# Performance work log

Measured on AMD Instinct MI355X. Metric: run time of the kernel, lower is better.

## Reference

```python
import jax, jax.numpy as jnp
import numpy as np

LOG2PI = float(np.log(2.0 * np.pi))

# Each Gaussian g is exp(-0.5*(a_g.x + b_g.y + c_g)^2)/sqrt(2*pi), with x the H current
# hidden variables and y the H next hidden variables. The original module applies a
# precompiled sequence of Givens-rotation 'gaussian products' (sequence_phase_1/2) that
# (phase 1) zero the x-coefficients of all but one pivot Gaussian per variable and
# integrate the pivots out, then (phase 2) rotate the leftover Gaussians so only H of
# them depend on y; leftover pure-bias Gaussians contribute norm_log_gaussian(bias).
# A sequence of Givens rotations is an orthogonal transform of the rows [a|b|c], so the
# whole procedure equals (up to per-row signs, which leave every Gaussian invariant):
#   QR on A -> integrate H pivots: LC1 = -sum_j log|R1_jj|
#   project B,c onto A's orthogonal complement, QR on PB -> kept rows (R2, Q2^T Pc)
#   residual bias energy -> LC2 = -0.5*((K-H)*log(2pi) + ||(P - Q2 Q2^T) c||^2)


def setup_inputs() -> dict:
    B, P, H, K, D = 2048, 4, 16, 48, 4
    key = jax.random.key(0)
    ks = jax.random.split(key, 8)
    f32 = jnp.float32
    return {
        "input_i": jax.random.normal(ks[0], (B, P, D), dtype=f32),
        "Prev_coefs": jax.random.normal(ks[1], (H, B, P, H), dtype=f32),
        "Prev_biases": jax.random.normal(ks[2], (H, B, P), dtype=f32),
        "LP": jnp.zeros((B, P), dtype=f32),
        "Log_factors": jax.random.normal(ks[3], (B, P), dtype=f32),
        "obs_var_coefs": jax.random.normal(ks[4], (K, B, P, D), dtype=f32),
        "hidden_var_coefs": jax.random.normal(ks[5], (K, B, P, H), dtype=f32),
        "next_hidden_var_coefs": jax.random.normal(ks[6], (K, B, P, H), dtype=f32),
        "rec_biases": jax.random.normal(ks[7], (K, B, P), dtype=f32),
    }


def reference(input_i, Prev_coefs, Prev_biases, LP, Log_factors,
              obs_var_coefs, hidden_var_coefs, next_hidden_var_coefs, rec_biases):
    H = Prev_coefs.shape[0]
    K = rec_biases.shape[0]
    # observation contribution to the recurrent Gaussians' biases: [K,B,P]
    cur_b = rec_biases + jnp.sum(obs_var_coefs * input_i[None], axis=-1)
    # stack all G = H + K Gaussians: coefs on current hidden vars (A), next hidden
    # vars (Bm) and biases (c). Previous-step Gaussians have zero next-var coefs.
    A = jnp.concatenate([Prev_coefs, hidden_var_coefs], axis=0)            # [G,B,P,H]
    Bm = jnp.concatenate([jnp.zeros_like(Prev_coefs), next_hidden_var_coefs], 0)
    c = jnp.concatenate([Prev_biases, cur_b], axis=0)                      # [G,B,P]
    A = jnp.moveaxis(A, 0, 2)   # [B,P,G,H]
    Bm = jnp.moveaxis(Bm, 0, 2)  # [B,P,G,H]
    c = jnp.moveaxis(c, 0, 2)   # [B,P,G]

    # phase 1: orthogonal elimination of the current-hidden-variable coefficients,
    # then integrate the H pivot Gaussians out.
    Q1, R1 = jnp.linalg.qr(A)                                              # Q1 [B,P,G,H]
    diag1 = jnp.abs(jnp.diagonal(R1, axis1=-2, axis2=-1))
    LC = -jnp.sum(jnp.log(diag1), axis=-1)                                 # [B,P]
    # project next-var coefs and biases onto the orthogonal complement of span(A)
    PB = Bm - Q1 @ (jnp.swapaxes(Q1, -1, -2) @ Bm)                         # [B,P,G,H]
    Pc = c - jnp.einsum('bpgh,bph->bpg', Q1, jnp.einsum('bpgh,bpg->bph', Q1, c))

    # phase 2: reduce the remaining K Gaussians to H kept ones.
    Q2, R2 = jnp.linalg.qr(PB)                                             # R2 [B,P,H,H]
    nb = jnp.einsum('bpgh,bpg->bph', Q2, Pc)                               # kept biases
    resid = jnp.maximum(jnp.sum(Pc * Pc, -1) - jnp.sum(nb * nb, -1), 0.0)
    # leftover (K - H) pure-bias Gaussians: sum of norm_log_gaussian(bias)
    LC = LC - 0.5 * ((K - H) * LOG2PI + resid)

    LP_new = LP + LC + Log_factors
    Next_coefs = jnp.moveaxis(R2, 2, 0)    # [H,B,P,H]
    Next_biases = jnp.moveaxis(nb, -1, 0)  # [H,B,P]
    return (Next_coefs, Next_biases, LP_new)
```

## Files before the change

kernel.cpp:

```cpp
#include <hip/hip_runtime.h>

#define LOG2PI 1.8378770664093453

__device__ __forceinline__ float rl32(float v, int l) {
  return __int_as_float(__builtin_amdgcn_readlane(__float_as_int(v), l));
}

#define OFF_M33   0
#define OFF_STAB  1188
#define OFF_T     1188
#define OFF_Y     1508
#define OFF_Z     1828
#define OFF_G     2148
#define OFF_CTOP  2454
#define OFF_ATOPT 2470
#define OFF_M2    2790
#define LDSZ      2792

__device__ __forceinline__ void slot_to_rq(int s, int& r, int& q) {
  if      (s < 4)   { r = s;               q = 0;    }
  else if (s < 12)  { int i=s-4;   r=4 +i/2; q=i-(i/2)*2; }
  else if (s < 24)  { int i=s-12;  r=8 +i/3; q=i-(i/3)*3; }
  else if (s < 40)  { int i=s-24;  r=12+(i>>2); q=i&3; }
  else if (s < 60)  { int i=s-40;  r=16+i/5; q=i-(i/5)*5; }
  else if (s < 84)  { int i=s-60;  r=20+i/6; q=i-(i/6)*6; }
  else if (s < 112) { int i=s-84;  r=24+i/7; q=i-(i/7)*7; }
  else if (s < 144) { int i=s-112; r=28+(i>>3); q=i&7; }
  else              { r = 32; q = s-144; }
}

__global__ __launch_bounds__(128, 7) void cint_kernel(
    const float* __restrict__ input_i,
    const float* __restrict__ Prev_coefs,
    const float* __restrict__ Prev_biases,
    const float* __restrict__ LPin,
    const float* __restrict__ Log_factors,
    const float* __restrict__ obs_var,
    const float* __restrict__ hid_var,
    const float* __restrict__ nxt_var,
    const float* __restrict__ rec_biases,
    float* __restrict__ out,
    int NBP)
{
  __shared__ float lds[LDSZ];

  const int tid  = threadIdx.x;
  const int w    = tid >> 6;
  const int lane = tid & 63;
  const int bid  = blockIdx.x;
  const int inst = (bid & 7) * (NBP >> 3) + (bid >> 3);

  const size_t NB_OFFv = (size_t)NBP * 256;
  const size_t LP_OFFv = NB_OFFv + (size_t)NBP * 16;

  const float lp_lf = LPin[inst] + Log_factors[inst];

  {
    const int g = lane;
    const size_t rowidx = (g < 16) ? ((size_t)g * NBP + inst)
                                   : ((size_t)(g - 16) * NBP + inst);
    if (w == 0) {
      const float* aptr = (g < 16) ? (Prev_coefs + rowidx * 16)
                                   : (hid_var    + rowidx * 16);
      float4 a0 = *(const float4*)(aptr + 0);
      float4 a1 = *(const float4*)(aptr + 4);
      float4 a2 = *(const float4*)(aptr + 8);
      float4 a3 = *(const float4*)(aptr + 12);
      *(float4*)&lds[g*36 +  0] = a0;
      *(float4*)&lds[g*36 +  4] = a1;
      *(float4*)&lds[g*36 +  8] = a2;
      *(float4*)&lds[g*36 + 12] = a3;
      if (g < 16) {
        lds[OFF_ATOPT +  0*20+g]=a0.x; lds[OFF_ATOPT +  1*20+g]=a0.y;
        lds[OFF_ATOPT +  2*20+g]=a0.z; lds[OFF_ATOPT +  3*20+g]=a0.w;
        lds[OFF_ATOPT +  4*20+g]=a1.x; lds[OFF_ATOPT +  5*20+g]=a1.y;
        lds[OFF_ATOPT +  6*20+g]=a1.z; lds[OFF_ATOPT +  7*20+g]=a1.w;
        lds[OFF_ATOPT +  8*20+g]=a2.x; lds[OFF_ATOPT +  9*20+g]=a2.y;
        lds[OFF_ATOPT + 10*20+g]=a2.z; lds[OFF_ATOPT + 11*20+g]=a2.w;
        lds[OFF_ATOPT + 12*20+g]=a3.x; lds[OFF_ATOPT + 13*20+g]=a3.y;
        lds[OFF_ATOPT + 14*20+g]=a3.z; lds[OFF_ATOPT + 15*20+g]=a3.w;
      }
    } else {
      float4 z4 = make_float4(0.f, 0.f, 0.f, 0.f);
      float4 b0 = z4, b1 = z4, b2 = z4, b3 = z4;
      float cv;
      if (g < 16) {
        cv = Prev_biases[rowidx];
        lds[OFF_CTOP + g] = cv;
      } else {
        const float* bptr = nxt_var + rowidx * 16;
        b0 = *(const float4*)(bptr + 0);
        b1 = *(const float4*)(bptr + 4);
        b2 = *(const float4*)(bptr + 8);
        b3 = *(const float4*)(bptr + 12);
        float4 ob = *(const float4*)(obs_var + rowidx * 4);
        float4 iv = *(const float4*)(input_i + (size_t)inst * 4);
        cv = rec_biases[rowidx] + ob.x*iv.x + ob.y*iv.y + ob.z*iv.z + ob.w*iv.w;
      }
      *(float4*)&lds[g*36 + 16] = b0;
      *(float4*)&lds[g*36 + 20] = b1;
      *(float4*)&lds[g*36 + 24] = b2;
      *(float4*)&lds[g*36 + 28] = b3;
      lds[g*36 + 32] = cv;
      lds[g*36 + 33] = 0.f; lds[g*36 + 34] = 0.f; lds[g*36 + 35] = 0.f;
    }
  }
  __syncthreads();

  int r0, q0; slot_to_rq(tid, r0, q0);
  float a00=0,a01=0,a02=0,a03=0;
  {
    #pragma unroll 8
    for (int g = 0; g < 64; ++g) {
      const float* xr = &lds[g*36];
      float  xi = xr[r0];
      float4 cv = *(const float4*)(xr + 4*q0);
      a00=fmaf(xi,cv.x,a00); a01=fmaf(xi,cv.y,a01);
      a02=fmaf(xi,cv.z,a02); a03=fmaf(xi,cv.w,a03);
    }
  }
  const bool has2 = (tid >= 103);
  int r1=0, q1=0;
  float a10=0,a11=0,a12=0,a13=0;
  if (has2) {
    slot_to_rq(tid + 25, r1, q1);
    #pragma unroll 8
    for (int g = 0; g < 64; ++g) {
      const float* xr = &lds[g*36];
      float  xi = xr[r1];
      float4 cv = *(const float4*)(xr + 4*q1);
      a10=fmaf(xi,cv.x,a10); a11=fmaf(xi,cv.y,a11);
      a12=fmaf(xi,cv.z,a12); a13=fmaf(xi,cv.w,a13);
    }
  }
  __syncthreads();

  {
    float4 v0 = make_float4(a00,a01,a02,a03);
    *(float4*)&lds[OFF_M33 + r0*36 + 4*q0] = v0;
    if (r0 >= 16 && q0 < 4) {
      const int k = r0 - 16;
      lds[OFF_STAB + (4*q0+0)*20 + k] = a00;
      lds[OFF_STAB + (4*q0+1)*20 + k] = a01;
      lds[OFF_STAB + (4*q0+2)*20 + k] = a02;
      lds[OFF_STAB + (4*q0+3)*20 + k] = a03;
    }
    if (has2) {
      float4 v1 = make_float4(a10,a11,a12,a13);
      *(float4*)&lds[OFF_M33 + r1*36 + 4*q1] = v1;
      if (r1 >= 16 && q1 < 4) {
        const int k = r1 - 16;
        lds[OFF_STAB + (4*q1+0)*20 + k] = a10;
        lds[OFF_STAB + (4*q1+1)*20 + k] = a11;
        lds[OFF_STAB + (4*q1+2)*20 + k] = a12;
        lds[OFF_STAB + (4*q1+3)*20 + k] = a13;
      }
    }
  }
  __syncthreads();

  if (w == 0) {
    float Lr[16];
    {
      const int ir = lane & 15;
      double prodd = 1.0;
      #pragma unroll
      for (int j = 0; j < 16; ++j) {
        float s = lds[OFF_M33 + ((ir >= j) ? (ir*36 + j) : (j*36 + ir))];
        #pragma unroll
        for (int m = 0; m < j; ++m) s = fmaf(-Lr[m], rl32(Lr[m], j), s);
        float sj = fmaxf(rl32(s, j), 1e-30f);
        float Ljj = sqrtf(sj);
        float iv  = 1.0f / Ljj;
        prodd *= (double)sj;
        Lr[j] = (ir == j) ? Ljj : s * iv;
        if (lane == j) lds[OFF_M33 + j*36 + 33] = iv;
      }
      if (lane == 0) lds[OFF_M2 + 1] = (float)(-0.5 * log(prodd));
    }
    {
      const bool isY = (lane < 17);
      const int  ci  = isY ? lane : ((lane - 17 < 15) ? lane - 17 : 15);
      const float* ip = isY ? &lds[OFF_STAB + ci] : &lds[OFF_ATOPT + ci];
      float x[16];
      #pragma unroll
      for (int j = 0; j < 16; ++j) {
        float t = ip[j*20];
        #pragma unroll
        for (int m = 0; m < j; ++m) t = fmaf(-rl32(Lr[m], j), x[m], t);
        x[j] = t * lds[OFF_M33 + j*36 + 33];
      }
      if (lane < 33) {
        float* op = isY ? &lds[OFF_Y + ci] : &lds[OFF_Z + ci];
        #pragma unroll
        for (int m = 0; m < 16; ++m) op[m*20] = x[m];
      }
    }
  }
  __syncthreads();

  for (int s = tid; s < 153; s += 128) {
    float fs = 8.f * (float)s + 1.f;
    int k = (int)((sqrtf(fs) - 1.f) * 0.5f);
    int l = s - ((k * (k + 1)) >> 1);
    float acc = lds[OFF_M33 + (16 + k)*36 + 16 + l];
    #pragma unroll
    for (int m = 0; m < 16; ++m)
      acc = fmaf(-lds[OFF_Y + m*20 + k], lds[OFF_Y + m*20 + l], acc);
    lds[OFF_G + k*18 + l] = acc;
    lds[OFF_G + l*18 + k] = acc;
  }
  {
    #pragma unroll
    for (int p = 0; p < 4; ++p) {
      int s = p * 128 + tid;
      int r  = s >> 5;
      int kk = s & 31;
      if (kk < 17) {
        float acc = (kk == 16) ? lds[OFF_CTOP + r] : 0.f;
        #pragma unroll
        for (int m = 0; m < 16; ++m)
          acc = fmaf(-lds[OFF_Z + m*20 + r], lds[OFF_Y + m*20 + kk], acc);
        lds[OFF_T + r*20 + kk] = acc;
      }
    }
  }
  __syncthreads();

  if (w == 0) {
    const int k  = lane;
    const int kc = (k < 17) ? k : 16;
    float Tr[16];
    float Gh[16];
    #pragma unroll
    for (int r = 0; r < 16; ++r) Tr[r] = lds[OFF_T + r*20 + kc];
    #pragma unroll
    for (int j = 0; j < 16; ++j) Gh[j] = lds[OFF_G + j*18 + kc];
    float nbacc = 0.0f;
    #pragma unroll
    for (int j = 0; j < 16; ++j) {
      float alf  = rl32(Tr[j], j);
      float nrm2 = rl32(Gh[j], j);
      float nrm  = sqrtf(fmaxf(nrm2, 1e-30f));
      float aa   = fabsf(alf);
      float tau  = 1.0f + aa / nrm;
      float inv  = copysignf(1.0f / (aa + nrm), alf);
      float beta = -copysignf(nrm, alf);
      float Tj   = Tr[j];
      float wv   = Tj + (Gh[j] - alf * Tj) * inv;
      float Rv   = Tj - tau * wv;
      if (k < 16) {
        float ov = (k < j) ? 0.0f : ((k == j) ? beta : Rv);
        out[((size_t)j * NBP + inst) * 16 + k] = ov;
      } else if (k == 16) {
        out[NB_OFFv + (size_t)j * NBP + inst] = Rv;
        nbacc = fmaf(Rv, Rv, nbacc);
      }
      float twi = tau * wv * inv;
      #pragma unroll
      for (int r = j + 1; r < 16; ++r) {
        float vr = rl32(Tr[r], j);
        Tr[r] = fmaf(-twi, vr, Tr[r]);
      }
      #pragma unroll
      for (int l = j + 1; l < 16; ++l) {
        float Rl = rl32(Rv, l);
        Gh[l] = fmaf(-Rl, Rv, Gh[l]);
      }
    }
    if (k == 16) {
      double resid = fmax((double)lds[OFF_G + 16*18 + 16] - (double)nbacc, 0.0);
      double LC = (double)lds[OFF_M2 + 1] - 0.5 * (32.0 * LOG2PI + resid);
      out[LP_OFFv + (size_t)inst] = lp_lf + (float)LC;
    }
  }
}

extern "C" void kernel_launch(void* const* d_in, const int* in_sizes, int n_in,
                              void* d_out, int out_size, void* d_ws, size_t ws_size,
                              hipStream_t stream) {
  (void)n_in; (void)out_size; (void)d_ws; (void)ws_size;
  const int NBP = in_sizes[3];
  cint_kernel<<<NBP, 128, 0, stream>>>(
      (const float*)d_in[0], (const float*)d_in[1], (const float*)d_in[2],
      (const float*)d_in[3], (const float*)d_in[4], (const float*)d_in[5],
      (const float*)d_in[6], (const float*)d_in[7], (const float*)d_in[8],
      (float*)d_out, NBP);
}
```

Measured before the change: 177.0 us.

## Collapse per-instance block to a single wavefront and drop all barriers

Each instance is now handled by one 64-lane wavefront instead of two, so every __syncthreads is removed. Each lane computes up to three Gram-matrix slots instead of one or two. The LDS layout is compacted by reusing the Gram region for the T and G intermediates and reading transposed inputs in place instead of staging copies. The intent is to cut barrier and idle-wave overhead, at the cost of more serial work per wave, lower launch_bounds occupancy and correctness that now depends on lockstep wave execution for LDS visibility.

```diff
diff --git a/kernel.cpp b/kernel.cpp
--- a/kernel.cpp
+++ b/kernel.cpp
@@ -6,16 +6,11 @@
   return __int_as_float(__builtin_amdgcn_readlane(__float_as_int(v), l));
 }
 
-#define OFF_M33   0
-#define OFF_STAB  1188
-#define OFF_T     1188
-#define OFF_Y     1508
-#define OFF_Z     1828
-#define OFF_G     2148
-#define OFF_CTOP  2454
-#define OFF_ATOPT 2470
-#define OFF_M2    2790
-#define LDSZ      2792
+#define MO   1116
+#define YO   2304
+#define ZO   2576
+#define LC1O (MO + 34)
+#define WSZ  2848
 
 __device__ __forceinline__ void slot_to_rq(int s, int& r, int& q) {
   if      (s < 4)   { r = s;               q = 0;    }
@@ -29,7 +24,7 @@
   else              { r = 32; q = s-144; }
 }
 
-__global__ __launch_bounds__(128, 7) void cint_kernel(
+__global__ __launch_bounds__(64, 4) void cint_kernel(
     const float* __restrict__ input_i,
     const float* __restrict__ Prev_coefs,
     const float* __restrict__ Prev_biases,
@@ -42,11 +37,9 @@
     float* __restrict__ out,
     int NBP)
 {
-  __shared__ float lds[LDSZ];
-
-  const int tid  = threadIdx.x;
-  const int w    = tid >> 6;
-  const int lane = tid & 63;
+  __shared__ float L[WSZ];
+
+  const int lane = threadIdx.x;
   const int bid  = blockIdx.x;
   const int inst = (bid & 7) * (NBP >> 3) + (bid >> 3);
 
@@ -57,185 +50,134 @@
 
   {
     const int g = lane;
-    const size_t rowidx = (g < 16) ? ((size_t)g * NBP + inst)
-                                   : ((size_t)(g - 16) * NBP + inst);
-    if (w == 0) {
-      const float* aptr = (g < 16) ? (Prev_coefs + rowidx * 16)
-                                   : (hid_var    + rowidx * 16);
-      float4 a0 = *(const float4*)(aptr + 0);
-      float4 a1 = *(const float4*)(aptr + 4);
-      float4 a2 = *(const float4*)(aptr + 8);
-      float4 a3 = *(const float4*)(aptr + 12);
-      *(float4*)&lds[g*36 +  0] = a0;
-      *(float4*)&lds[g*36 +  4] = a1;
-      *(float4*)&lds[g*36 +  8] = a2;
-      *(float4*)&lds[g*36 + 12] = a3;
-      if (g < 16) {
-        lds[OFF_ATOPT +  0*20+g]=a0.x; lds[OFF_ATOPT +  1*20+g]=a0.y;
-        lds[OFF_ATOPT +  2*20+g]=a0.z; lds[OFF_ATOPT +  3*20+g]=a0.w;
-        lds[OFF_ATOPT +  4*20+g]=a1.x; lds[OFF_ATOPT +  5*20+g]=a1.y;
-        lds[OFF_ATOPT +  6*20+g]=a1.z; lds[OFF_ATOPT +  7*20+g]=a1.w;
-        lds[OFF_ATOPT +  8*20+g]=a2.x; lds[OFF_ATOPT +  9*20+g]=a2.y;
-        lds[OFF_ATOPT + 10*20+g]=a2.z; lds[OFF_ATOPT + 11*20+g]=a2.w;
-        lds[OFF_ATOPT + 12*20+g]=a3.x; lds[OFF_ATOPT + 13*20+g]=a3.y;
-        lds[OFF_ATOPT + 14*20+g]=a3.z; lds[OFF_ATOPT + 15*20+g]=a3.w;
-      }
+    const size_t rowidx = ((size_t)(g < 16 ? g : g - 16)) * NBP + inst;
+    const float4 z4 = make_float4(0.f, 0.f, 0.f, 0.f);
+    if (g < 16) {
+      const float* aptr = Prev_coefs + rowidx * 16;
+      *(float4*)&L[g*36 +  0] = *(const float4*)(aptr + 0);
+      *(float4*)&L[g*36 +  4] = *(const float4*)(aptr + 4);
+      *(float4*)&L[g*36 +  8] = *(const float4*)(aptr + 8);
+      *(float4*)&L[g*36 + 12] = *(const float4*)(aptr + 12);
+      *(float4*)&L[g*36 + 16] = z4;
+      *(float4*)&L[g*36 + 20] = z4;
+      *(float4*)&L[g*36 + 24] = z4;
+      *(float4*)&L[g*36 + 28] = z4;
+      float c = Prev_biases[rowidx];
+      *(float4*)&L[g*36 + 32] = make_float4(c, 0.f, 0.f, 0.f);
     } else {
-      float4 z4 = make_float4(0.f, 0.f, 0.f, 0.f);
-      float4 b0 = z4, b1 = z4, b2 = z4, b3 = z4;
-      float cv;
-      if (g < 16) {
-        cv = Prev_biases[rowidx];
-        lds[OFF_CTOP + g] = cv;
-      } else {
-        const float* bptr = nxt_var + rowidx * 16;
-        b0 = *(const float4*)(bptr + 0);
-        b1 = *(const float4*)(bptr + 4);
-        b2 = *(const float4*)(bptr + 8);
-        b3 = *(const float4*)(bptr + 12);
-        float4 ob = *(const float4*)(obs_var + rowidx * 4);
-        float4 iv = *(const float4*)(input_i + (size_t)inst * 4);
-        cv = rec_biases[rowidx] + ob.x*iv.x + ob.y*iv.y + ob.z*iv.z + ob.w*iv.w;
-      }
-      *(float4*)&lds[g*36 + 16] = b0;
-      *(float4*)&lds[g*36 + 20] = b1;
-      *(float4*)&lds[g*36 + 24] = b2;
-      *(float4*)&lds[g*36 + 28] = b3;
-      lds[g*36 + 32] = cv;
-      lds[g*36 + 33] = 0.f; lds[g*36 + 34] = 0.f; lds[g*36 + 35] = 0.f;
-    }
-  }
-  __syncthreads();
-
-  int r0, q0; slot_to_rq(tid, r0, q0);
-  float a00=0,a01=0,a02=0,a03=0;
-  {
-    #pragma unroll 8
+      const float* aptr = hid_var + rowidx * 16;
+      *(float4*)&L[g*36 +  0] = *(const float4*)(aptr + 0);
+      *(float4*)&L[g*36 +  4] = *(const float4*)(aptr + 4);
+      *(float4*)&L[g*36 +  8] = *(const float4*)(aptr + 8);
+      *(float4*)&L[g*36 + 12] = *(const float4*)(aptr + 12);
+      const float* bptr = nxt_var + rowidx * 16;
+      *(float4*)&L[g*36 + 16] = *(const float4*)(bptr + 0);
+      *(float4*)&L[g*36 + 20] = *(const float4*)(bptr + 4);
+      *(float4*)&L[g*36 + 24] = *(const float4*)(bptr + 8);
+      *(float4*)&L[g*36 + 28] = *(const float4*)(bptr + 12);
+      float4 ob = *(const float4*)(obs_var + rowidx * 4);
+      float4 iv = *(const float4*)(input_i + (size_t)inst * 4);
+      float c = rec_biases[rowidx] + ob.x*iv.x + ob.y*iv.y + ob.z*iv.z + ob.w*iv.w;
+      *(float4*)&L[g*36 + 32] = make_float4(c, 0.f, 0.f, 0.f);
+    }
+  }
+
+  {
+    int r0,q0,r1,q1,r2,q2;
+    slot_to_rq(lane,      r0, q0);
+    slot_to_rq(lane + 64, r1, q1);
+    const bool h3 = (lane < 25);
+    slot_to_rq(h3 ? lane + 128 : 152, r2, q2);
+    float a00=0,a01=0,a02=0,a03=0;
+    float a10=0,a11=0,a12=0,a13=0;
+    float a20=0,a21=0,a22=0,a23=0;
+    #pragma unroll 4
     for (int g = 0; g < 64; ++g) {
-      const float* xr = &lds[g*36];
-      float  xi = xr[r0];
-      float4 cv = *(const float4*)(xr + 4*q0);
-      a00=fmaf(xi,cv.x,a00); a01=fmaf(xi,cv.y,a01);
-      a02=fmaf(xi,cv.z,a02); a03=fmaf(xi,cv.w,a03);
-    }
-  }
-  const bool has2 = (tid >= 103);
-  int r1=0, q1=0;
-  float a10=0,a11=0,a12=0,a13=0;
-  if (has2) {
-    slot_to_rq(tid + 25, r1, q1);
-    #pragma unroll 8
-    for (int g = 0; g < 64; ++g) {
-      const float* xr = &lds[g*36];
-      float  xi = xr[r1];
-      float4 cv = *(const float4*)(xr + 4*q1);
-      a10=fmaf(xi,cv.x,a10); a11=fmaf(xi,cv.y,a11);
-      a12=fmaf(xi,cv.z,a12); a13=fmaf(xi,cv.w,a13);
-    }
-  }
-  __syncthreads();
-
-  {
-    float4 v0 = make_float4(a00,a01,a02,a03);
-    *(float4*)&lds[OFF_M33 + r0*36 + 4*q0] = v0;
-    if (r0 >= 16 && q0 < 4) {
-      const int k = r0 - 16;
-      lds[OFF_STAB + (4*q0+0)*20 + k] = a00;
-      lds[OFF_STAB + (4*q0+1)*20 + k] = a01;
-      lds[OFF_STAB + (4*q0+2)*20 + k] = a02;
-      lds[OFF_STAB + (4*q0+3)*20 + k] = a03;
-    }
-    if (has2) {
-      float4 v1 = make_float4(a10,a11,a12,a13);
-      *(float4*)&lds[OFF_M33 + r1*36 + 4*q1] = v1;
-      if (r1 >= 16 && q1 < 4) {
-        const int k = r1 - 16;
-        lds[OFF_STAB + (4*q1+0)*20 + k] = a10;
-        lds[OFF_STAB + (4*q1+1)*20 + k] = a11;
-        lds[OFF_STAB + (4*q1+2)*20 + k] = a12;
-        lds[OFF_STAB + (4*q1+3)*20 + k] = a13;
-      }
-    }
-  }
-  __syncthreads();
-
-  if (w == 0) {
-    float Lr[16];
-    {
-      const int ir = lane & 15;
-      double prodd = 1.0;
-      #pragma unroll
-      for (int j = 0; j < 16; ++j) {
-        float s = lds[OFF_M33 + ((ir >= j) ? (ir*36 + j) : (j*36 + ir))];
-        #pragma unroll
-        for (int m = 0; m < j; ++m) s = fmaf(-Lr[m], rl32(Lr[m], j), s);
-        float sj = fmaxf(rl32(s, j), 1e-30f);
-        float Ljj = sqrtf(sj);
-        float iv  = 1.0f / Ljj;
-        prodd *= (double)sj;
-        Lr[j] = (ir == j) ? Ljj : s * iv;
-        if (lane == j) lds[OFF_M33 + j*36 + 33] = iv;
-      }
-      if (lane == 0) lds[OFF_M2 + 1] = (float)(-0.5 * log(prodd));
-    }
-    {
-      const bool isY = (lane < 17);
-      const int  ci  = isY ? lane : ((lane - 17 < 15) ? lane - 17 : 15);
-      const float* ip = isY ? &lds[OFF_STAB + ci] : &lds[OFF_ATOPT + ci];
-      float x[16];
-      #pragma unroll
-      for (int j = 0; j < 16; ++j) {
-        float t = ip[j*20];
-        #pragma unroll
-        for (int m = 0; m < j; ++m) t = fmaf(-rl32(Lr[m], j), x[m], t);
-        x[j] = t * lds[OFF_M33 + j*36 + 33];
-      }
-      if (lane < 33) {
-        float* op = isY ? &lds[OFF_Y + ci] : &lds[OFF_Z + ci];
-        #pragma unroll
-        for (int m = 0; m < 16; ++m) op[m*20] = x[m];
-      }
-    }
-  }
-  __syncthreads();
-
-  for (int s = tid; s < 153; s += 128) {
+      const float* xr = &L[g*36];
+      float  x0 = xr[r0]; float4 v0 = *(const float4*)(xr + 4*q0);
+      float  x1 = xr[r1]; float4 v1 = *(const float4*)(xr + 4*q1);
+      float  x2 = xr[r2]; float4 v2 = *(const float4*)(xr + 4*q2);
+      a00=fmaf(x0,v0.x,a00); a01=fmaf(x0,v0.y,a01);
+      a02=fmaf(x0,v0.z,a02); a03=fmaf(x0,v0.w,a03);
+      a10=fmaf(x1,v1.x,a10); a11=fmaf(x1,v1.y,a11);
+      a12=fmaf(x1,v1.z,a12); a13=fmaf(x1,v1.w,a13);
+      a20=fmaf(x2,v2.x,a20); a21=fmaf(x2,v2.y,a21);
+      a22=fmaf(x2,v2.z,a22); a23=fmaf(x2,v2.w,a23);
+    }
+    *(float4*)&L[MO + r0*36 + 4*q0] = make_float4(a00,a01,a02,a03);
+    *(float4*)&L[MO + r1*36 + 4*q1] = make_float4(a10,a11,a12,a13);
+    if (h3)
+      *(float4*)&L[MO + r2*36 + 4*q2] = make_float4(a20,a21,a22,a23);
+  }
+
+  float Lr[16];
+  {
+    const int ir = lane & 15;
+    double prodd = 1.0;
+    #pragma unroll
+    for (int j = 0; j < 16; ++j) {
+      float s = L[MO + ((ir >= j) ? (ir*36 + j) : (j*36 + ir))];
+      #pragma unroll
+      for (int m = 0; m < j; ++m) s = fmaf(-Lr[m], rl32(Lr[m], j), s);
+      float sj = fmaxf(rl32(s, j), 1e-30f);
+      float Ljj = sqrtf(sj);
+      float iv  = 1.0f / Ljj;
+      prodd *= (double)sj;
+      Lr[j] = (ir == j) ? Ljj : s * iv;
+      if (lane == j) L[MO + j*36 + 33] = iv;
+    }
+    if (lane == 0) L[LC1O] = (float)(-0.5 * log(prodd));
+  }
+
+  {
+    const bool isY = (lane < 17);
+    const int  ci  = isY ? lane : ((lane - 17 < 15) ? lane - 17 : 15);
+    float x[16];
+    #pragma unroll
+    for (int j = 0; j < 16; ++j) {
+      float t = isY ? L[MO + (16 + ci)*36 + j] : L[ci*36 + j];
+      #pragma unroll
+      for (int m = 0; m < j; ++m) t = fmaf(-rl32(Lr[m], j), x[m], t);
+      x[j] = t * L[MO + j*36 + 33];
+    }
+    if (lane < 33) {
+      float* op = isY ? &L[YO + ci] : &L[ZO + ci];
+      #pragma unroll
+      for (int m = 0; m < 16; ++m) op[m*17] = x[m];
+    }
+  }
+
+  for (int s = lane; s < 153; s += 64) {
     float fs = 8.f * (float)s + 1.f;
     int k = (int)((sqrtf(fs) - 1.f) * 0.5f);
     int l = s - ((k * (k + 1)) >> 1);
-    float acc = lds[OFF_M33 + (16 + k)*36 + 16 + l];
+    float acc = L[MO + (16 + k)*36 + 16 + l];
     #pragma unroll
     for (int m = 0; m < 16; ++m)
-      acc = fmaf(-lds[OFF_Y + m*20 + k], lds[OFF_Y + m*20 + l], acc);
-    lds[OFF_G + k*18 + l] = acc;
-    lds[OFF_G + l*18 + k] = acc;
-  }
-  {
-    #pragma unroll
-    for (int p = 0; p < 4; ++p) {
-      int s = p * 128 + tid;
-      int r  = s >> 5;
-      int kk = s & 31;
-      if (kk < 17) {
-        float acc = (kk == 16) ? lds[OFF_CTOP + r] : 0.f;
-        #pragma unroll
-        for (int m = 0; m < 16; ++m)
-          acc = fmaf(-lds[OFF_Z + m*20 + r], lds[OFF_Y + m*20 + kk], acc);
-        lds[OFF_T + r*20 + kk] = acc;
-      }
-    }
-  }
-  __syncthreads();
-
-  if (w == 0) {
+      acc = fmaf(-L[YO + m*17 + k], L[YO + m*17 + l], acc);
+    L[MO + (16 + k)*36 + 16 + l] = acc;
+    L[MO + (16 + l)*36 + 16 + k] = acc;
+  }
+
+  for (int s = lane; s < 272; s += 64) {
+    int r = s / 17;
+    int k = s - r * 17;
+    float acc = (k == 16) ? L[r*36 + 32] : 0.f;
+    #pragma unroll
+    for (int m = 0; m < 16; ++m)
+      acc = fmaf(-L[ZO + m*17 + r], L[YO + m*17 + k], acc);
+    L[MO + r*36 + k] = acc;
+  }
+
+  {
     const int k  = lane;
     const int kc = (k < 17) ? k : 16;
     float Tr[16];
     float Gh[16];
     #pragma unroll
-    for (int r = 0; r < 16; ++r) Tr[r] = lds[OFF_T + r*20 + kc];
-    #pragma unroll
-    for (int j = 0; j < 16; ++j) Gh[j] = lds[OFF_G + j*18 + kc];
+    for (int r = 0; r < 16; ++r) Tr[r] = L[MO + r*36 + kc];
+    #pragma unroll
+    for (int j = 0; j < 16; ++j) Gh[j] = L[MO + (16 + j)*36 + 16 + kc];
     float nbacc = 0.0f;
     #pragma unroll
     for (int j = 0; j < 16; ++j) {
@@ -269,8 +211,8 @@
       }
     }
     if (k == 16) {
-      double resid = fmax((double)lds[OFF_G + 16*18 + 16] - (double)nbacc, 0.0);
-      double LC = (double)lds[OFF_M2 + 1] - 0.5 * (32.0 * LOG2PI + resid);
+      double resid = fmax((double)L[MO + 32*36 + 32] - (double)nbacc, 0.0);
+      double LC = (double)L[LC1O] - 0.5 * (32.0 * LOG2PI + resid);
       out[LP_OFFv + (size_t)inst] = lp_lf + (float)LC;
     }
   }
@@ -281,7 +223,7 @@
                               hipStream_t stream) {
   (void)n_in; (void)out_size; (void)d_ws; (void)ws_size;
   const int NBP = in_sizes[3];
-  cint_kernel<<<NBP, 128, 0, stream>>>(
+  cint_kernel<<<NBP, 64, 0, stream>>>(
       (const float*)d_in[0], (const float*)d_in[1], (const float*)d_in[2],
       (const float*)d_in[3], (const float*)d_in[4], (const float*)d_in[5],
       (const float*)d_in[6], (const float*)d_in[7], (const float*)d_in[8],
```

Measured after the change: 169.9 us. -4.0%, faster.
